# Kernel optimization log

Hardware: AMD Instinct MI355X
Metric: run time of the kernel (lower is better)

Reference implementation:

```python
import jax, jax.numpy as jnp
import numpy as np

BETA = 0.95
THR = 0.8
SLOPE = 25.0  # fast_sigmoid surrogate slope


@jax.custom_vjp
def spike(x):
    # Heaviside forward, fast-sigmoid surrogate backward (snntorch surrogate.fast_sigmoid)
    return (x > 0).astype(x.dtype)

def _spike_fwd(x):
    return spike(x), x

def _spike_bwd(x, g):
    return (g / (SLOPE * jnp.abs(x) + 1.0) ** 2,)

spike.defvjp(_spike_fwd, _spike_bwd)


def setup_inputs() -> dict:
    key = jax.random.key(0)
    k1, k2, k3 = jax.random.split(key, 3)
    B, T, D, H, C = 512, 2000, 20, 128, 10
    x = jax.random.normal(k1, (B, T, D), dtype=jnp.float32)
    # kaiming_normal_ with nonlinearity='linear': std = 1/sqrt(fan_in)
    W1 = jax.random.normal(k2, (H, D), dtype=jnp.float32) / np.sqrt(D)
    b1 = jnp.zeros((H,), jnp.float32)
    W2 = jax.random.normal(k3, (C, H), dtype=jnp.float32) / np.sqrt(H)
    b2 = jnp.zeros((C,), jnp.float32)
    return {"x": x, "W1": W1, "b1": b1, "W2": W2, "b2": b2}


def reference(x, W1, b1, W2, b2):
    B, T, D = x.shape
    H = W1.shape[0]

    def step(mem, xt):
        cur = xt @ W1.T + b1                                  # [B,H]
        # snntorch Leaky: reset based on PREVIOUS mem (detached), subtract mechanism
        reset = jax.lax.stop_gradient(spike(mem - THR))
        mem_new = BETA * mem + cur - reset * THR
        spk = spike(mem_new - THR)
        return mem_new, spk

    mem0 = jnp.zeros((B, H), x.dtype)
    _, spks = jax.lax.scan(step, mem0, jnp.swapaxes(x, 0, 1))  # spks: [T,B,H]

    spikeCounts = spks.sum(0)                                  # [B,H]
    # sum_t fc2(spk_t) = spikeCounts @ W2^T + T * b2
    logits = (spikeCounts @ W2.T + T * b2) / T
    logits = logits + 0.1 * ((spikeCounts / (T + 1e-6)) @ W2.T + b2)
    return logits
```

## Files before the change

kernel.cpp:

```cpp
#include <hip/hip_runtime.h>
#include <stdint.h>

#define Bdim 512
#define Tdim 2000
#define Ddim 20
#define Hdim 128
#define Cdim 10
#define TT   64
#define NCH  32
#define BETA 0.95f
#define THR  0.8f

typedef float f32x2 __attribute__((ext_vector_type(2)));
typedef float f32x4 __attribute__((ext_vector_type(4)));
typedef int   i32x4 __attribute__((ext_vector_type(4)));

#define CVT_HILO(HI, LO, F0, F1) {                                                     \
    asm volatile("v_cvt_pk_bf16_f32 %0, %1, %2" : "=v"(HI) : "v"(F0), "v"(F1));        \
    const float h0f_ = __uint_as_float((HI) << 16);                                    \
    const float h1f_ = __uint_as_float((HI) & 0xFFFF0000u);                            \
    const float l0_ = (F0) - h0f_;  const float l1_ = (F1) - h1f_;                     \
    asm volatile("v_cvt_pk_bf16_f32 %0, %1, %2" : "=v"(LO) : "v"(l0_), "v"(l1_)); }

#define MFMA0(ACC, A8, B8) \
  asm volatile("v_mfma_f32_16x16x32_bf16 %0, %1, %2, 0"  : "=v"(ACC) : "v"(A8), "v"(B8));
#define MFMA(ACC, A8, B8)  \
  asm volatile("v_mfma_f32_16x16x32_bf16 %0, %1, %2, %0" : "+v"(ACC) : "v"(A8), "v"(B8));

__global__ __launch_bounds__(256, 1) void snn_spec_kernel(
    const float* __restrict__ x,
    const float* __restrict__ W1,
    const float* __restrict__ b1,
    const float* __restrict__ W2,
    const float* __restrict__ b2,
    float* __restrict__ out)
{
  const int b   = blockIdx.x;
  const int tid = threadIdx.x;
  const int wid = tid >> 6;
  const int l   = tid & 63;
  const int r   = l & 15;
  const int g   = l >> 4;

  __shared__ __align__(16) float xraw[2][TT * Ddim];
  __shared__ __align__(16) float cur[2][TT * 132];
  __shared__ float cnt_s[Hdim];

  const float* xb = x + (size_t)b * (Tdim * Ddim);
  const float* const clampMax = x + (size_t)Bdim * Tdim * Ddim - 4;

  const uint32_t xrawB = (uint32_t)(uintptr_t)&xraw[0][0];
  const uint32_t curB  = (uint32_t)(uintptr_t)&cur[0][0];

  i32x4 bhi[8], blo[8];
  f32x4 zero4, ovr;
  bool  sel23 = false, g3f = false;
  if (wid < 2) {
    const bool g2 = (g == 2);
    g3f   = (g == 3);
    sel23 = g2 | g3f;
    zero4[0]=0.f; zero4[1]=0.f; zero4[2]=0.f; zero4[3]=0.f;
    ovr = zero4; if (g2) ovr[0] = 1.0f;
#pragma unroll
    for (int ni = 0; ni < 8; ++ni) {
      const int hh = ni * 16 + r;
      float wv[8];
#pragma unroll
      for (int j = 0; j < 8; ++j) {
        const int k = 8 * g + j;
        wv[j] = (k < Ddim) ? W1[hh * Ddim + k] : ((k == Ddim) ? b1[hh] : 0.0f);
      }
#pragma unroll
      for (int d = 0; d < 4; ++d) {
        const uint32_t u0 = __float_as_uint(wv[2*d]), u1 = __float_as_uint(wv[2*d+1]);
        const uint32_t h0 = (u0 + 0x8000u) & 0xFFFF0000u;
        const uint32_t h1 = (u1 + 0x8000u) & 0xFFFF0000u;
        bhi[ni][d] = (int)(h1 | (h0 >> 16));
        const float l0 = wv[2*d]   - __uint_as_float(h0);
        const float l1 = wv[2*d+1] - __uint_as_float(h1);
        const uint32_t e0 = (__float_as_uint(l0) + 0x8000u) & 0xFFFF0000u;
        const uint32_t e1 = (__float_as_uint(l1) + 0x8000u) & 0xFFFF0000u;
        blo[ni][d] = (int)(e1 | (e0 >> 16));
      }
    }
  }

  float    mem = 0.0f;
  bool     sp  = false;
  uint32_t cnt = 0u;
  f32x2    negT2; negT2[0] = -THR; negT2[1] = -THR;
  const int sid = wid - 2;

#define STAGE(CH, BUF) do {                                                            \
    const float* g0_ = xb + (CH) * 1280 + wid * 640 + l * 4;                           \
    char* lb_ = (char*)&xraw[0][0] + (BUF) * 5120 + wid * 2560 + l * 16;               \
    const float* p0_ = g0_;        if (p0_ > clampMax) p0_ = clampMax;                 \
    const float* p1_ = g0_ + 256;  if (p1_ > clampMax) p1_ = clampMax;                 \
    __builtin_amdgcn_global_load_lds(                                                  \
      (const __attribute__((address_space(1))) unsigned int*)p0_,                      \
      (__attribute__((address_space(3))) unsigned int*)lb_, 16, 0, 0);                 \
    __builtin_amdgcn_global_load_lds(                                                  \
      (const __attribute__((address_space(1))) unsigned int*)p1_,                      \
      (__attribute__((address_space(3))) unsigned int*)(lb_ + 1024), 16, 0, 0);        \
    if (l < 32) {                                                                      \
      const float* p2_ = g0_ + 512;  if (p2_ > clampMax) p2_ = clampMax;               \
      __builtin_amdgcn_global_load_lds(                                                \
        (const __attribute__((address_space(1))) unsigned int*)p2_,                    \
        (__attribute__((address_space(3))) unsigned int*)(lb_ + 2048), 16, 0, 0);      \
    } } while (0)

#define GEMM_MT(MIDX) {                                                                \
    const int mt_ = 2 * wid + (MIDX);                                                  \
    const uint32_t afb_ = xrawB + (uint32_t)(pbuf * 5120 + mt_ * 1280 + 80 * r + 32 * g); \
    f32x4 a0_, a1_;                                                                    \
    asm volatile("ds_read_b128 %0, %1 offset:0"  : "=v"(a0_) : "v"(afb_));             \
    asm volatile("ds_read_b128 %0, %1 offset:16" : "=v"(a1_) : "v"(afb_));             \
    asm volatile("s_waitcnt lgkmcnt(0)" ::: "memory");                                 \
    __builtin_amdgcn_sched_barrier(0);                                                 \
    a0_ = g3f   ? zero4 : a0_;                                                         \
    a1_ = sel23 ? ovr   : a1_;                                                         \
    i32x4 ahi_, alo_;                                                                  \
    { uint32_t h_, lo_;                                                                \
      CVT_HILO(h_, lo_, a0_[0], a0_[1]) ahi_[0]=(int)h_; alo_[0]=(int)lo_;             \
      CVT_HILO(h_, lo_, a0_[2], a0_[3]) ahi_[1]=(int)h_; alo_[1]=(int)lo_;             \
      CVT_HILO(h_, lo_, a1_[0], a1_[1]) ahi_[2]=(int)h_; alo_[2]=(int)lo_;             \
      CVT_HILO(h_, lo_, a1_[2], a1_[3]) ahi_[3]=(int)h_; alo_[3]=(int)lo_; }           \
    asm volatile("s_nop 2");                                                           \
    f32x4 ac0,ac1,ac2,ac3,ac4,ac5,ac6,ac7;                                             \
    MFMA0(ac0, alo_, bhi[0]) MFMA0(ac1, alo_, bhi[1]) MFMA0(ac2, alo_, bhi[2])         \
    MFMA0(ac3, alo_, bhi[3]) MFMA0(ac4, alo_, bhi[4]) MFMA0(ac5, alo_, bhi[5])         \
    MFMA0(ac6, alo_, bhi[6]) MFMA0(ac7, alo_, bhi[7])                                  \
    MFMA (ac0, ahi_, blo[0]) MFMA (ac1, ahi_, blo[1]) MFMA (ac2, ahi_, blo[2])         \
    MFMA (ac3, ahi_, blo[3]) MFMA (ac4, ahi_, blo[4]) MFMA (ac5, ahi_, blo[5])         \
    MFMA (ac6, ahi_, blo[6]) MFMA (ac7, ahi_, blo[7])                                  \
    MFMA (ac0, ahi_, bhi[0]) MFMA (ac1, ahi_, bhi[1]) MFMA (ac2, ahi_, bhi[2])         \
    MFMA (ac3, ahi_, bhi[3]) MFMA (ac4, ahi_, bhi[4]) MFMA (ac5, ahi_, bhi[5])         \
    MFMA (ac6, ahi_, bhi[6]) MFMA (ac7, ahi_, bhi[7])                                  \
    asm volatile("s_nop 7"); asm volatile("s_nop 4");                                  \
    const uint32_t cwb_  = curB + (uint32_t)(pbuf * 33792 + 528 * (mt_ * 16 + 4 * g) + 4 * r); \
    const uint32_t cwb2_ = cwb_ + 1056u;                                               \
    CW2(0, ac0) CW2(1, ac1) CW2(2, ac2) CW2(3, ac3)                                    \
    CW2(4, ac4) CW2(5, ac5) CW2(6, ac6) CW2(7, ac7) }

#define CW2(NI, AC)                                                                    \
    asm volatile("ds_write2_b32 %0, %1, %2 offset0:%c3 offset1:%c4"                    \
                 :: "v"(cwb_),  "v"(AC[0]), "v"(AC[1]), "n"(16*(NI)), "n"(16*(NI)+132)); \
    asm volatile("ds_write2_b32 %0, %1, %2 offset0:%c3 offset1:%c4"                    \
                 :: "v"(cwb2_), "v"(AC[2]), "v"(AC[3]), "n"(16*(NI)), "n"(16*(NI)+132));

#define RD2(PR, AD) asm volatile("ds_read2_b32 %0, %1 offset0:0 offset1:132" : "=v"(PR) : "v"(AD));
#define LGW(N) asm volatile("s_waitcnt lgkmcnt(" #N ")" ::: "memory"); __builtin_amdgcn_sched_barrier(0);
#define CONSUME(PR) {                                                                  \
    f32x2 cm_; asm("v_pk_add_f32 %0, %1, %2" : "=v"(cm_) : "v"(PR), "v"(negT2));       \
    float mP_ = fmaf(BETA, mem, PR[0]);                                                \
    float mM_ = fmaf(BETA, mem, cm_[0]);                                               \
    mem = sp ? mM_ : mP_;                                                              \
    sp  = mem > THR;                                                                   \
    cnt += sp ? 1u : 0u;                                                               \
    mP_ = fmaf(BETA, mem, PR[1]);                                                      \
    mM_ = fmaf(BETA, mem, cm_[1]);                                                     \
    mem = sp ? mM_ : mP_;                                                              \
    sp  = mem > THR;                                                                   \
    cnt += sp ? 1u : 0u; }
#define SSLOT(S) { LGW(7) CONSUME(pr##S) a##S += 8448u; RD2(pr##S, a##S) }
#define TSLOT(S, W) { LGW(W) CONSUME(pr##S) }
#define SCAN_PRO()                                                                     \
    uint32_t a0 = spB, a1 = spB+1056u, a2 = spB+2112u, a3 = spB+3168u,                 \
             a4 = spB+4224u, a5 = spB+5280u, a6 = spB+6336u, a7 = spB+7392u;           \
    f32x2 pr0, pr1, pr2, pr3, pr4, pr5, pr6, pr7;                                      \
    RD2(pr0,a0) RD2(pr1,a1) RD2(pr2,a2) RD2(pr3,a3)                                    \
    RD2(pr4,a4) RD2(pr5,a5) RD2(pr6,a6) RD2(pr7,a7)
#define SCAN_TAIL8()                                                                   \
    TSLOT(0,7) TSLOT(1,6) TSLOT(2,5) TSLOT(3,4)                                        \
    TSLOT(4,3) TSLOT(5,2) TSLOT(6,1) TSLOT(7,0)

  if (wid < 2) STAGE(0, 0);

#pragma unroll 1
  for (int ph = 0; ph <= NCH; ++ph) {
    if (wid < 2) {
      if (ph <= NCH - 1) {
        asm volatile("s_waitcnt vmcnt(0)" ::: "memory");
        if (ph < NCH - 1) STAGE(ph + 1, (ph + 1) & 1);
        const int pbuf = ph & 1;
        if (ph < NCH - 1) {
          GEMM_MT(0)
          GEMM_MT(1)
        } else if (wid == 0) {
          GEMM_MT(0)
        }
        asm volatile("s_waitcnt lgkmcnt(0)" ::: "memory");
      }
    } else {
      if (ph >= 1) {
        const uint32_t spB = curB + (uint32_t)(((ph - 1) & 1) * 33792 + 4 * (sid * 64 + l));
        if (ph - 1 < NCH - 1) {
          SCAN_PRO()
          SSLOT(0) SSLOT(1) SSLOT(2) SSLOT(3) SSLOT(4) SSLOT(5) SSLOT(6) SSLOT(7)
          SSLOT(0) SSLOT(1) SSLOT(2) SSLOT(3) SSLOT(4) SSLOT(5) SSLOT(6) SSLOT(7)
          SSLOT(0) SSLOT(1) SSLOT(2) SSLOT(3) SSLOT(4) SSLOT(5) SSLOT(6) SSLOT(7)
          SCAN_TAIL8()
        } else {
          SCAN_PRO()
          SCAN_TAIL8()
        }
        if (ph == NCH) cnt_s[sid * 64 + l] = (float)cnt;
      }
    }
    __syncthreads();
  }

  if (tid < Cdim) {
    float dot = 0.0f;
#pragma unroll
    for (int k = 0; k < Hdim; ++k)
      dot = fmaf(cnt_s[k], W2[tid * Hdim + k], dot);
    const float Tf = (float)Tdim;
    const float scale = 1.0f / Tf + 0.1f / (Tf + 1e-6f);
    out[b * Cdim + tid] = fmaf(dot, scale, 1.1f * b2[tid]);
  }
}

extern "C" void kernel_launch(void* const* d_in, const int* in_sizes, int n_in,
                              void* d_out, int out_size, void* d_ws, size_t ws_size,
                              hipStream_t stream) {
  const float* x  = (const float*)d_in[0];
  const float* W1 = (const float*)d_in[1];
  const float* b1 = (const float*)d_in[2];
  const float* W2 = (const float*)d_in[3];
  const float* b2 = (const float*)d_in[4];
  float* out = (float*)d_out;

  snn_spec_kernel<<<dim3(Bdim), dim3(256), 0, stream>>>(x, W1, b1, W2, b2, out);
}
```

Baseline: 62.20 us.

## Fuse GEMM and scan into same waves with interleaved software pipeline

Replaces the producer/consumer split (2 GEMM waves plus 2 scan waves, 256 threads) with 128 threads where each wave computes input currents for its own 64 hidden units via MFMA and runs the recurrent scan for those units. The MFMA tile work for the next chunk is interleaved with the LIF scan of the previous chunk, and the cur buffer is split per wave so only a lightweight s_barrier is needed. The goal is to hide MFMA latency behind the serial scan and use half the threads per block. The trade-off is higher register pressure and a more intricate hand-scheduled pipeline with explicit prologue and epilogue stages.

Result: slower. 79.86 us (+28.4%).

```diff
diff --git a/kernel.cpp b/kernel.cpp
--- a/kernel.cpp
+++ b/kernel.cpp
@@ -6,7 +6,6 @@
 #define Ddim 20
 #define Hdim 128
 #define Cdim 10
-#define TT   64
 #define NCH  32
 #define BETA 0.95f
 #define THR  0.8f
@@ -27,7 +26,7 @@
 #define MFMA(ACC, A8, B8)  \
   asm volatile("v_mfma_f32_16x16x32_bf16 %0, %1, %2, %0" : "+v"(ACC) : "v"(A8), "v"(B8));
 
-__global__ __launch_bounds__(256, 1) void snn_spec_kernel(
+__global__ __launch_bounds__(128, 1) void snn_fuse3_kernel(
     const float* __restrict__ x,
     const float* __restrict__ W1,
     const float* __restrict__ b1,
@@ -42,46 +41,41 @@
   const int r   = l & 15;
   const int g   = l >> 4;
 
-  __shared__ __align__(16) float xraw[2][TT * Ddim];
-  __shared__ __align__(16) float cur[2][TT * 132];
+  __shared__ __align__(16) float xraw[2][1280];
+  __shared__ __align__(16) float cur[2][2][64 * 66];
   __shared__ float cnt_s[Hdim];
 
   const float* xb = x + (size_t)b * (Tdim * Ddim);
   const float* const clampMax = x + (size_t)Bdim * Tdim * Ddim - 4;
 
   const uint32_t xrawB = (uint32_t)(uintptr_t)&xraw[0][0];
-  const uint32_t curB  = (uint32_t)(uintptr_t)&cur[0][0];
-
-  i32x4 bhi[8], blo[8];
+  const uint32_t curB  = (uint32_t)(uintptr_t)&cur[0][0][0];
+
+  i32x4 bhi[4], blo[4];
   f32x4 zero4, ovr;
-  bool  sel23 = false, g3f = false;
-  if (wid < 2) {
-    const bool g2 = (g == 2);
-    g3f   = (g == 3);
-    sel23 = g2 | g3f;
-    zero4[0]=0.f; zero4[1]=0.f; zero4[2]=0.f; zero4[3]=0.f;
-    ovr = zero4; if (g2) ovr[0] = 1.0f;
-#pragma unroll
-    for (int ni = 0; ni < 8; ++ni) {
-      const int hh = ni * 16 + r;
-      float wv[8];
-#pragma unroll
-      for (int j = 0; j < 8; ++j) {
-        const int k = 8 * g + j;
-        wv[j] = (k < Ddim) ? W1[hh * Ddim + k] : ((k == Ddim) ? b1[hh] : 0.0f);
-      }
-#pragma unroll
-      for (int d = 0; d < 4; ++d) {
-        const uint32_t u0 = __float_as_uint(wv[2*d]), u1 = __float_as_uint(wv[2*d+1]);
-        const uint32_t h0 = (u0 + 0x8000u) & 0xFFFF0000u;
-        const uint32_t h1 = (u1 + 0x8000u) & 0xFFFF0000u;
-        bhi[ni][d] = (int)(h1 | (h0 >> 16));
-        const float l0 = wv[2*d]   - __uint_as_float(h0);
-        const float l1 = wv[2*d+1] - __uint_as_float(h1);
-        const uint32_t e0 = (__float_as_uint(l0) + 0x8000u) & 0xFFFF0000u;
-        const uint32_t e1 = (__float_as_uint(l1) + 0x8000u) & 0xFFFF0000u;
-        blo[ni][d] = (int)(e1 | (e0 >> 16));
-      }
+  const bool g2 = (g == 2), g3f = (g == 3), sel23 = g2 | g3f;
+  zero4[0]=0.f; zero4[1]=0.f; zero4[2]=0.f; zero4[3]=0.f;
+  ovr = zero4; if (g2) ovr[0] = 1.0f;
+#pragma unroll
+  for (int ni = 0; ni < 4; ++ni) {
+    const int hh = (wid << 6) + ni * 16 + r;
+    float wv[8];
+#pragma unroll
+    for (int j = 0; j < 8; ++j) {
+      const int k = 8 * g + j;
+      wv[j] = (k < Ddim) ? W1[hh * Ddim + k] : ((k == Ddim) ? b1[hh] : 0.0f);
+    }
+#pragma unroll
+    for (int d = 0; d < 4; ++d) {
+      const uint32_t u0 = __float_as_uint(wv[2*d]), u1 = __float_as_uint(wv[2*d+1]);
+      const uint32_t h0 = (u0 + 0x8000u) & 0xFFFF0000u;
+      const uint32_t h1 = (u1 + 0x8000u) & 0xFFFF0000u;
+      bhi[ni][d] = (int)(h1 | (h0 >> 16));
+      const float l0 = wv[2*d]   - __uint_as_float(h0);
+      const float l1 = wv[2*d+1] - __uint_as_float(h1);
+      const uint32_t e0 = (__float_as_uint(l0) + 0x8000u) & 0xFFFF0000u;
+      const uint32_t e1 = (__float_as_uint(l1) + 0x8000u) & 0xFFFF0000u;
+      blo[ni][d] = (int)(e1 | (e0 >> 16));
     }
   }
 
@@ -89,7 +83,6 @@
   bool     sp  = false;
   uint32_t cnt = 0u;
   f32x2    negT2; negT2[0] = -THR; negT2[1] = -THR;
-  const int sid = wid - 2;
 
 #define STAGE(CH, BUF) do {                                                            \
     const float* g0_ = xb + (CH) * 1280 + wid * 640 + l * 4;                           \
@@ -109,47 +102,53 @@
         (__attribute__((address_space(3))) unsigned int*)(lb_ + 2048), 16, 0, 0);      \
     } } while (0)
 
-#define GEMM_MT(MIDX) {                                                                \
-    const int mt_ = 2 * wid + (MIDX);                                                  \
-    const uint32_t afb_ = xrawB + (uint32_t)(pbuf * 5120 + mt_ * 1280 + 80 * r + 32 * g); \
-    f32x4 a0_, a1_;                                                                    \
-    asm volatile("ds_read_b128 %0, %1 offset:0"  : "=v"(a0_) : "v"(afb_));             \
-    asm volatile("ds_read_b128 %0, %1 offset:16" : "=v"(a1_) : "v"(afb_));             \
-    asm volatile("s_waitcnt lgkmcnt(0)" ::: "memory");                                 \
-    __builtin_amdgcn_sched_barrier(0);                                                 \
+#define VM0()  asm volatile("s_waitcnt vmcnt(0)" ::: "memory");
+#define LGW(N) asm volatile("s_waitcnt lgkmcnt(" #N ")" ::: "memory"); __builtin_amdgcn_sched_barrier(0);
+#define BAR()  __builtin_amdgcn_sched_barrier(0); __builtin_amdgcn_s_barrier(); __builtin_amdgcn_sched_barrier(0);
+
+#define CVT8(AHI, ALO, A0, A1) {                                                       \
+    uint32_t h_, lo_;                                                                  \
+    CVT_HILO(h_, lo_, A0[0], A0[1]) AHI[0]=(int)h_; ALO[0]=(int)lo_;                   \
+    CVT_HILO(h_, lo_, A0[2], A0[3]) AHI[1]=(int)h_; ALO[1]=(int)lo_;                   \
+    CVT_HILO(h_, lo_, A1[0], A1[1]) AHI[2]=(int)h_; ALO[2]=(int)lo_;                   \
+    CVT_HILO(h_, lo_, A1[2], A1[3]) AHI[3]=(int)h_; ALO[3]=(int)lo_; }
+
+#define ARD8()                                                                         \
+  asm volatile("ds_read_b128 %0, %1 offset:0"    : "=v"(ax00) : "v"(afb));             \
+  asm volatile("ds_read_b128 %0, %1 offset:16"   : "=v"(ax01) : "v"(afb));             \
+  asm volatile("ds_read_b128 %0, %1 offset:1280" : "=v"(ax10) : "v"(afb));             \
+  asm volatile("ds_read_b128 %0, %1 offset:1296" : "=v"(ax11) : "v"(afb));             \
+  asm volatile("ds_read_b128 %0, %1 offset:2560" : "=v"(ax20) : "v"(afb));             \
+  asm volatile("ds_read_b128 %0, %1 offset:2576" : "=v"(ax21) : "v"(afb));             \
+  asm volatile("ds_read_b128 %0, %1 offset:3840" : "=v"(ax30) : "v"(afb));             \
+  asm volatile("ds_read_b128 %0, %1 offset:3856" : "=v"(ax31) : "v"(afb));
+#define ARD2()                                                                         \
+  asm volatile("ds_read_b128 %0, %1 offset:0"    : "=v"(ax00) : "v"(afb));             \
+  asm volatile("ds_read_b128 %0, %1 offset:16"   : "=v"(ax01) : "v"(afb));
+
+#define TILE(MT) {                                                                     \
+    f32x4 a0_ = ax##MT##0, a1_ = ax##MT##1;                                            \
     a0_ = g3f   ? zero4 : a0_;                                                         \
     a1_ = sel23 ? ovr   : a1_;                                                         \
-    i32x4 ahi_, alo_;                                                                  \
-    { uint32_t h_, lo_;                                                                \
-      CVT_HILO(h_, lo_, a0_[0], a0_[1]) ahi_[0]=(int)h_; alo_[0]=(int)lo_;             \
-      CVT_HILO(h_, lo_, a0_[2], a0_[3]) ahi_[1]=(int)h_; alo_[1]=(int)lo_;             \
-      CVT_HILO(h_, lo_, a1_[0], a1_[1]) ahi_[2]=(int)h_; alo_[2]=(int)lo_;             \
-      CVT_HILO(h_, lo_, a1_[2], a1_[3]) ahi_[3]=(int)h_; alo_[3]=(int)lo_; }           \
+    i32x4 ahi_, alo_;  CVT8(ahi_, alo_, a0_, a1_)                                      \
     asm volatile("s_nop 2");                                                           \
-    f32x4 ac0,ac1,ac2,ac3,ac4,ac5,ac6,ac7;                                             \
-    MFMA0(ac0, alo_, bhi[0]) MFMA0(ac1, alo_, bhi[1]) MFMA0(ac2, alo_, bhi[2])         \
-    MFMA0(ac3, alo_, bhi[3]) MFMA0(ac4, alo_, bhi[4]) MFMA0(ac5, alo_, bhi[5])         \
-    MFMA0(ac6, alo_, bhi[6]) MFMA0(ac7, alo_, bhi[7])                                  \
-    MFMA (ac0, ahi_, blo[0]) MFMA (ac1, ahi_, blo[1]) MFMA (ac2, ahi_, blo[2])         \
-    MFMA (ac3, ahi_, blo[3]) MFMA (ac4, ahi_, blo[4]) MFMA (ac5, ahi_, blo[5])         \
-    MFMA (ac6, ahi_, blo[6]) MFMA (ac7, ahi_, blo[7])                                  \
-    MFMA (ac0, ahi_, bhi[0]) MFMA (ac1, ahi_, bhi[1]) MFMA (ac2, ahi_, bhi[2])         \
-    MFMA (ac3, ahi_, bhi[3]) MFMA (ac4, ahi_, bhi[4]) MFMA (ac5, ahi_, bhi[5])         \
-    MFMA (ac6, ahi_, bhi[6]) MFMA (ac7, ahi_, bhi[7])                                  \
-    asm volatile("s_nop 7"); asm volatile("s_nop 4");                                  \
-    const uint32_t cwb_  = curB + (uint32_t)(pbuf * 33792 + 528 * (mt_ * 16 + 4 * g) + 4 * r); \
-    const uint32_t cwb2_ = cwb_ + 1056u;                                               \
-    CW2(0, ac0) CW2(1, ac1) CW2(2, ac2) CW2(3, ac3)                                    \
-    CW2(4, ac4) CW2(5, ac5) CW2(6, ac6) CW2(7, ac7) }
-
-#define CW2(NI, AC)                                                                    \
+    MFMA0(c##MT##_0, alo_, bhi[0]) MFMA0(c##MT##_1, alo_, bhi[1])                      \
+    MFMA0(c##MT##_2, alo_, bhi[2]) MFMA0(c##MT##_3, alo_, bhi[3])                      \
+    MFMA (c##MT##_0, ahi_, blo[0]) MFMA (c##MT##_1, ahi_, blo[1])                      \
+    MFMA (c##MT##_2, ahi_, blo[2]) MFMA (c##MT##_3, ahi_, blo[3])                      \
+    MFMA (c##MT##_0, ahi_, bhi[0]) MFMA (c##MT##_1, ahi_, bhi[1])                      \
+    MFMA (c##MT##_2, ahi_, bhi[2]) MFMA (c##MT##_3, ahi_, bhi[3]) }
+
+#define WT1(CW, ACC, NI)                                                               \
     asm volatile("ds_write2_b32 %0, %1, %2 offset0:%c3 offset1:%c4"                    \
-                 :: "v"(cwb_),  "v"(AC[0]), "v"(AC[1]), "n"(16*(NI)), "n"(16*(NI)+132)); \
+                 :: "v"(CW), "v"(ACC[0]), "v"(ACC[1]), "n"(16*(NI)), "n"(16*(NI)+66)); \
     asm volatile("ds_write2_b32 %0, %1, %2 offset0:%c3 offset1:%c4"                    \
-                 :: "v"(cwb2_), "v"(AC[2]), "v"(AC[3]), "n"(16*(NI)), "n"(16*(NI)+132));
-
-#define RD2(PR, AD) asm volatile("ds_read2_b32 %0, %1 offset0:0 offset1:132" : "=v"(PR) : "v"(AD));
-#define LGW(N) asm volatile("s_waitcnt lgkmcnt(" #N ")" ::: "memory"); __builtin_amdgcn_sched_barrier(0);
+                 :: "v"(CW), "v"(ACC[2]), "v"(ACC[3]), "n"(16*(NI)+132), "n"(16*(NI)+198));
+#define WTILE(MT) { const uint32_t cw_ = cwb + (MT) * (16u * 264u);                    \
+    WT1(cw_, c##MT##_0, 0) WT1(cw_, c##MT##_1, 1)                                      \
+    WT1(cw_, c##MT##_2, 2) WT1(cw_, c##MT##_3, 3) }
+
+#define RD2A(PR, AD) asm volatile("ds_read2_b32 %0, %1 offset0:0 offset1:66" : "=v"(PR) : "v"(AD));
 #define CONSUME(PR) {                                                                  \
     f32x2 cm_; asm("v_pk_add_f32 %0, %1, %2" : "=v"(cm_) : "v"(PR), "v"(negT2));       \
     float mP_ = fmaf(BETA, mem, PR[0]);                                                \
@@ -162,53 +161,86 @@
     mem = sp ? mM_ : mP_;                                                              \
     sp  = mem > THR;                                                                   \
     cnt += sp ? 1u : 0u; }
-#define SSLOT(S) { LGW(7) CONSUME(pr##S) a##S += 8448u; RD2(pr##S, a##S) }
-#define TSLOT(S, W) { LGW(W) CONSUME(pr##S) }
-#define SCAN_PRO()                                                                     \
-    uint32_t a0 = spB, a1 = spB+1056u, a2 = spB+2112u, a3 = spB+3168u,                 \
-             a4 = spB+4224u, a5 = spB+5280u, a6 = spB+6336u, a7 = spB+7392u;           \
-    f32x2 pr0, pr1, pr2, pr3, pr4, pr5, pr6, pr7;                                      \
-    RD2(pr0,a0) RD2(pr1,a1) RD2(pr2,a2) RD2(pr3,a3)                                    \
-    RD2(pr4,a4) RD2(pr5,a5) RD2(pr6,a6) RD2(pr7,a7)
-#define SCAN_TAIL8()                                                                   \
-    TSLOT(0,7) TSLOT(1,6) TSLOT(2,5) TSLOT(3,4)                                        \
-    TSLOT(4,3) TSLOT(5,2) TSLOT(6,1) TSLOT(7,0)
-
-  if (wid < 2) STAGE(0, 0);
+#define SPRE()                                                                         \
+    f32x2 pr0, pr1, pr2, pr3, pr4, pr5, pr6;                                           \
+    RD2A(pr0, spB)         RD2A(pr1, spB + 528u)  RD2A(pr2, spB + 1056u)               \
+    RD2A(pr3, spB + 1584u) RD2A(pr4, spB + 2112u) RD2A(pr5, spB + 2640u)               \
+    RD2A(pr6, spB + 3168u)
+#define SSX(RG, SLOT) { LGW(6) CONSUME(pr##RG)                                         \
+    { const uint32_t ad_ = spB + (uint32_t)((SLOT) * 528u); RD2A(pr##RG, ad_) } }
+#define TSX(RG, W)    { LGW(W) CONSUME(pr##RG) }
+
+#define SCAN32_A()                                                      \
+    SSX(0,7)  SSX(1,8)  SSX(2,9)  SSX(3,10) SSX(4,11) SSX(5,12) SSX(6,13) SSX(0,14)
+#define SCAN32_B()                                                      \
+    SSX(1,15) SSX(2,16) SSX(3,17) SSX(4,18) SSX(5,19) SSX(6,20) SSX(0,21) SSX(1,22)
+#define SCAN32_C()                                                     \
+    SSX(2,23) SSX(3,24) SSX(4,25) SSX(5,26) SSX(6,27) SSX(0,28) SSX(1,29) SSX(2,30)
+#define SCAN32_D()                                                     \
+    SSX(3,31) TSX(4,6) TSX(5,5) TSX(6,4) TSX(0,3) TSX(1,2) TSX(2,1) TSX(3,0)
+
+  const uint32_t afb0 = xrawB + (uint32_t)(80 * r + 32 * g);
+  const uint32_t cwb0 = curB + (uint32_t)(wid * 33792 + (4 * g) * 264 + 4 * r);
+  const uint32_t spB0 = curB + (uint32_t)(wid * 33792 + 4 * l);
+
+  f32x4 ax00, ax01, ax10, ax11, ax20, ax21, ax30, ax31;
+  f32x4 c0_0,c0_1,c0_2,c0_3, c1_0,c1_1,c1_2,c1_3,
+        c2_0,c2_1,c2_2,c2_3, c3_0,c3_1,c3_2,c3_3;
+
+  STAGE(0, 0);
+
+  {
+    VM0() BAR()
+    STAGE(1, 1);
+    const uint32_t afb = afb0;
+    const uint32_t cwb = cwb0;
+    ARD8() LGW(0)
+    TILE(0) TILE(1) TILE(2) TILE(3)
+    asm volatile("s_nop 7"); asm volatile("s_nop 4");
+    WTILE(0) WTILE(1) WTILE(2) WTILE(3)
+    LGW(0)
+  }
 
 #pragma unroll 1
-  for (int ph = 0; ph <= NCH; ++ph) {
-    if (wid < 2) {
-      if (ph <= NCH - 1) {
-        asm volatile("s_waitcnt vmcnt(0)" ::: "memory");
-        if (ph < NCH - 1) STAGE(ph + 1, (ph + 1) & 1);
-        const int pbuf = ph & 1;
-        if (ph < NCH - 1) {
-          GEMM_MT(0)
-          GEMM_MT(1)
-        } else if (wid == 0) {
-          GEMM_MT(0)
-        }
-        asm volatile("s_waitcnt lgkmcnt(0)" ::: "memory");
-      }
-    } else {
-      if (ph >= 1) {
-        const uint32_t spB = curB + (uint32_t)(((ph - 1) & 1) * 33792 + 4 * (sid * 64 + l));
-        if (ph - 1 < NCH - 1) {
-          SCAN_PRO()
-          SSLOT(0) SSLOT(1) SSLOT(2) SSLOT(3) SSLOT(4) SSLOT(5) SSLOT(6) SSLOT(7)
-          SSLOT(0) SSLOT(1) SSLOT(2) SSLOT(3) SSLOT(4) SSLOT(5) SSLOT(6) SSLOT(7)
-          SSLOT(0) SSLOT(1) SSLOT(2) SSLOT(3) SSLOT(4) SSLOT(5) SSLOT(6) SSLOT(7)
-          SCAN_TAIL8()
-        } else {
-          SCAN_PRO()
-          SCAN_TAIL8()
-        }
-        if (ph == NCH) cnt_s[sid * 64 + l] = (float)cnt;
-      }
-    }
-    __syncthreads();
-  }
+  for (int ph = 1; ph <= 30; ++ph) {
+    VM0() BAR()
+    STAGE(ph + 1, (ph + 1) & 1);
+    const uint32_t pb  = (uint32_t)(ph & 1);
+    const uint32_t afb = afb0 + pb * 5120u;
+    const uint32_t cwb = cwb0 + pb * 16896u;
+    const uint32_t spB = spB0 + (1u - pb) * 16896u;
+    ARD8() SPRE()
+    LGW(7)
+    TILE(0) SCAN32_A()
+    TILE(1) SCAN32_B()
+    TILE(2) SCAN32_C()
+    TILE(3) SCAN32_D()
+    WTILE(0) WTILE(1) WTILE(2) WTILE(3)
+    LGW(0)
+  }
+
+  {
+    VM0() BAR()
+    const uint32_t afb = afb0 + 5120u;
+    const uint32_t cwb = cwb0 + 16896u;
+    const uint32_t spB = spB0;
+    ARD2() SPRE()
+    LGW(7)
+    TILE(0)
+    SCAN32_A() SCAN32_B() SCAN32_C() SCAN32_D()
+    WTILE(0)
+    LGW(0)
+  }
+
+  {
+    const uint32_t spB = spB0 + 16896u;
+    SPRE()
+    SSX(0,7)
+    TSX(1,6) TSX(2,5) TSX(3,4) TSX(4,3) TSX(5,2) TSX(6,1) TSX(0,0)
+  }
+
+  cnt_s[(wid << 6) + l] = (float)cnt;
+  __syncthreads();
 
   if (tid < Cdim) {
     float dot = 0.0f;
@@ -231,5 +263,5 @@
   const float* b2 = (const float*)d_in[4];
   float* out = (float*)d_out;
 
-  snn_spec_kernel<<<dim3(Bdim), dim3(256), 0, stream>>>(x, W1, b1, W2, b2, out);
+  snn_fuse3_kernel<<<dim3(Bdim), dim3(128), 0, stream>>>(x, W1, b1, W2, b2, out);
 }
```
